# Performance work log

Measured on AMD Instinct MI355X. Metric: run time of the kernel, lower is better.

Reference implementation:

```python
import jax, jax.numpy as jnp
import numpy as np

B, L, C = 2048, 2048, 16
F = L // 2                 # num_freqs = 1024
H = 4 * F                  # multi_factor * num_freqs = 4096
P = int(len(np.unique(L // np.arange(1, F + 1))))  # n patch sizes = 88
SCALE = 0.02
NOISE_EPS = 0.01


def setup_inputs() -> dict:
    key = jax.random.key(0)
    ks = jax.random.split(key, 10)
    return {
        "x": jax.random.normal(ks[0], (B, L, C), jnp.float32),
        "w_start": SCALE * jax.random.normal(ks[1], (C, 1), jnp.float32),
        "b_start": SCALE * jax.random.normal(ks[2], (1,), jnp.float32),
        "w1": SCALE * jax.random.normal(ks[3], (2, F, H), jnp.float32),
        "b1": SCALE * jax.random.normal(ks[4], (2, H), jnp.float32),
        "w2": SCALE * jax.random.normal(ks[5], (2, H, F), jnp.float32),
        "b2": SCALE * jax.random.normal(ks[6], (2, F), jnp.float32),
        "w_gate": SCALE * jax.random.normal(ks[7], (F, P), jnp.float32),
        "w_noise": SCALE * jax.random.normal(ks[8], (F, P), jnp.float32),
        "noise_z": jax.random.normal(ks[9], (B, P), jnp.float32),
        "top_k": 3,
    }


def reference(x, w_start, b_start, w1, b1, w2, b2, w_gate, w_noise, noise_z, top_k):
    # start_fc: [B, L, C] -> [B, L, 1] -> [B, 1, L]
    v = (jnp.einsum("blc,co->blo", x, w_start) + b_start).transpose(0, 2, 1)
    # rfft (ortho), drop DC bin -> [B, 1, F] complex
    xf = jnp.fft.rfft(v, axis=-1, norm="ortho")[:, :, 1:]
    xr, xi = jnp.real(xf), jnp.imag(xf)
    # complex 2-layer MLP in frequency domain
    o1r = jax.nn.relu(jnp.einsum("bdi,io->bdo", xr, w1[0]) - jnp.einsum("bdi,io->bdo", xi, w1[1]) + b1[0])
    o1i = jax.nn.relu(jnp.einsum("bdi,io->bdo", xi, w1[0]) + jnp.einsum("bdi,io->bdo", xr, w1[1]) + b1[1])
    o2r = jnp.einsum("bdo,of->bdf", o1r, w2[0]) - jnp.einsum("bdo,of->bdf", o1i, w2[1]) + b2[0]
    o2i = jnp.einsum("bdo,of->bdf", o1i, w2[0]) + jnp.einsum("bdo,of->bdf", o1r, w2[1]) + b2[1]
    amp = jnp.sqrt(o2r * o2r + o2i * o2i)[:, 0, :]  # [B, F]
    # router logits with (training) noise injection
    clean_logits = amp @ w_gate                      # [B, P]
    noise_std = jax.nn.softplus(amp @ w_noise) + NOISE_EPS
    logits = clean_logits + noise_z * noise_std
    # top-k -> softmax over top-k -> scatter into sparse gates
    top_w, top_i = jax.lax.top_k(logits, top_k)
    top_w = jax.nn.softmax(top_w, axis=-1)
    rows = jnp.arange(logits.shape[0])[:, None]
    gates = jnp.zeros_like(logits).at[rows, top_i].set(top_w)
    return gates
```

## Files before the change

### kernel.cpp

```cpp
#include <hip/hip_runtime.h>
#include <hip/hip_bf16.h>
#include <math.h>

#define B_DIM 2048
#define L_DIM 2048
#define F_DIM 1024
#define H_DIM 4096
#define P_DIM 88

typedef unsigned short u16;
typedef short bf16x8 __attribute__((ext_vector_type(8)));
typedef float f32x4 __attribute__((ext_vector_type(4)));

__device__ __forceinline__ u16 f2bf(float x) {
    unsigned u = __float_as_uint(x);
    return (u16)((u + 0x7fffu + ((u >> 16) & 1u)) >> 16);
}
__device__ __forceinline__ float bf2f(u16 h) {
    return __uint_as_float(((unsigned)h) << 16);
}

__device__ __forceinline__ void gload_lds16(const void* g, void* l) {
    unsigned loff = (unsigned)(uintptr_t)l;
    __builtin_amdgcn_global_load_lds(
        reinterpret_cast<const __attribute__((address_space(1))) void*>(
            reinterpret_cast<uintptr_t>(g)),
        reinterpret_cast<__attribute__((address_space(3))) void*>(loff),
        16, 0, 0);
}

__global__ __launch_bounds__(256) void fft_kernel(
    const float* __restrict__ x, const float* __restrict__ w_start,
    const float* __restrict__ b_start, u16* __restrict__ A1)
{
    __shared__ float re[2048];
    __shared__ float im[2048];
    __shared__ float twr[1024];
    __shared__ float twi[1024];
    int b = blockIdx.x;

    const float4* wp = (const float4*)w_start;
    float4 w0 = wp[0], w1 = wp[1], w2 = wp[2], w3 = wp[3];
    float bs = b_start[0];

    for (int i = threadIdx.x; i < 1024; i += 256) {
        float ang = -6.283185307179586f * ((float)i / 2048.0f);
        sincosf(ang, &twi[i], &twr[i]);
    }

    for (int l = threadIdx.x; l < 2048; l += 256) {
        const float4* xp = (const float4*)(x + ((size_t)b * 2048 + l) * 16);
        float4 x0 = xp[0], x1 = xp[1], x2 = xp[2], x3 = xp[3];
        float acc = bs;
        acc += x0.x * w0.x + x0.y * w0.y + x0.z * w0.z + x0.w * w0.w;
        acc += x1.x * w1.x + x1.y * w1.y + x1.z * w1.z + x1.w * w1.w;
        acc += x2.x * w2.x + x2.y * w2.y + x2.z * w2.z + x2.w * w2.w;
        acc += x3.x * w3.x + x3.y * w3.y + x3.z * w3.z + x3.w * w3.w;
        unsigned j = __brev((unsigned)l) >> 21;
        re[j] = acc;
        im[j] = 0.f;
    }
    __syncthreads();

    for (int s = 1; s <= 11; s++) {
        int half = 1 << (s - 1);
        for (int t = threadIdx.x; t < 1024; t += 256) {
            int j = t & (half - 1);
            int base = (t >> (s - 1)) << s;
            int idx = j << (11 - s);
            float wr = twr[idx], wi = twi[idx];
            int i0 = base + j, i1 = i0 + half;
            float br = re[i1], bi = im[i1];
            float tr = br * wr - bi * wi;
            float ti = br * wi + bi * wr;
            float ar = re[i0], ai = im[i0];
            re[i0] = ar + tr; im[i0] = ai + ti;
            re[i1] = ar - tr; im[i1] = ai - ti;
        }
        __syncthreads();
    }

    const float sc = 0.022097086912079612f;
    u16* arow = A1 + (size_t)b * 4096;
    for (int t = threadIdx.x; t < 1024; t += 256) {
        float r = re[t + 1] * sc;
        float q = im[t + 1] * sc;
        u16 rh = f2bf(r); u16 rl = f2bf(r - bf2f(rh));
        u16 ih = f2bf(q); u16 il = f2bf(q - bf2f(ih));
        arow[t] = rh; arow[1024 + t] = rl;
        arow[2048 + t] = ih; arow[3072 + t] = il;
    }
}

__global__ __launch_bounds__(256) void conv_bt_kernel(
    const float* __restrict__ w, u16* __restrict__ BT, int Kc, int Nh)
{
    __shared__ float t0[32][33];
    __shared__ float t1[32][33];
    int k0 = blockIdx.x * 32, n0 = blockIdx.y * 32;
    int tx = threadIdx.x, ty = threadIdx.y;
    const float* w0 = w;
    const float* w1 = w + (size_t)Kc * Nh;

#pragma unroll
    for (int i = 0; i < 4; i++) {
        int k = k0 + ty + 8 * i;
        t0[ty + 8 * i][tx] = w0[(size_t)k * Nh + n0 + tx];
        t1[ty + 8 * i][tx] = w1[(size_t)k * Nh + n0 + tx];
    }
    __syncthreads();

    size_t K4 = 4 * (size_t)Kc;
    int k = k0 + tx;
#pragma unroll
    for (int i = 0; i < 4; i++) {
        int nl = ty + 8 * i;
        int n = n0 + nl;
        float br = t0[tx][nl];
        float bi = t1[tx][nl];
        u16 brh = f2bf(br); u16 brl = f2bf(br - bf2f(brh));
        float nbi = -bi;
        u16 nih = f2bf(nbi); u16 nil = f2bf(nbi - bf2f(nih));
        u16 pih = f2bf(bi);  u16 pil = f2bf(bi - bf2f(pih));
        u16* rowr = BT + (size_t)n * K4;
        rowr[0 * Kc + k] = brh; rowr[1 * Kc + k] = brl;
        rowr[2 * Kc + k] = nih; rowr[3 * Kc + k] = nil;
        u16* rowi = BT + (size_t)(Nh + n) * K4;
        rowi[0 * Kc + k] = pih; rowi[1 * Kc + k] = pil;
        rowi[2 * Kc + k] = brh; rowi[3 * Kc + k] = brl;
    }
}

extern __shared__ char smem8p[];

#define MFMA16(ACC0, ACC1, ACC2, ACC3, A0, A1, A2, A3, B0, B1, B2, B3)           \
    ACC0[0] = __builtin_amdgcn_mfma_f32_16x16x32_bf16(A0, B0, ACC0[0], 0, 0, 0); \
    ACC0[1] = __builtin_amdgcn_mfma_f32_16x16x32_bf16(A0, B1, ACC0[1], 0, 0, 0); \
    ACC0[2] = __builtin_amdgcn_mfma_f32_16x16x32_bf16(A0, B2, ACC0[2], 0, 0, 0); \
    ACC0[3] = __builtin_amdgcn_mfma_f32_16x16x32_bf16(A0, B3, ACC0[3], 0, 0, 0); \
    ACC1[0] = __builtin_amdgcn_mfma_f32_16x16x32_bf16(A1, B0, ACC1[0], 0, 0, 0); \
    ACC1[1] = __builtin_amdgcn_mfma_f32_16x16x32_bf16(A1, B1, ACC1[1], 0, 0, 0); \
    ACC1[2] = __builtin_amdgcn_mfma_f32_16x16x32_bf16(A1, B2, ACC1[2], 0, 0, 0); \
    ACC1[3] = __builtin_amdgcn_mfma_f32_16x16x32_bf16(A1, B3, ACC1[3], 0, 0, 0); \
    ACC2[0] = __builtin_amdgcn_mfma_f32_16x16x32_bf16(A2, B0, ACC2[0], 0, 0, 0); \
    ACC2[1] = __builtin_amdgcn_mfma_f32_16x16x32_bf16(A2, B1, ACC2[1], 0, 0, 0); \
    ACC2[2] = __builtin_amdgcn_mfma_f32_16x16x32_bf16(A2, B2, ACC2[2], 0, 0, 0); \
    ACC2[3] = __builtin_amdgcn_mfma_f32_16x16x32_bf16(A2, B3, ACC2[3], 0, 0, 0); \
    ACC3[0] = __builtin_amdgcn_mfma_f32_16x16x32_bf16(A3, B0, ACC3[0], 0, 0, 0); \
    ACC3[1] = __builtin_amdgcn_mfma_f32_16x16x32_bf16(A3, B1, ACC3[1], 0, 0, 0); \
    ACC3[2] = __builtin_amdgcn_mfma_f32_16x16x32_bf16(A3, B2, ACC3[2], 0, 0, 0); \
    ACC3[3] = __builtin_amdgcn_mfma_f32_16x16x32_bf16(A3, B3, ACC3[3], 0, 0, 0);

template <int EPI, int SWZ>
__global__ __launch_bounds__(512, 2) void gemm8p(
    const u16* __restrict__ A, const u16* __restrict__ B,
    const float* __restrict__ biasL, const float* __restrict__ biasR,
    u16* __restrict__ OutU, float* __restrict__ P01, float* __restrict__ P23,
    int Kc, int KcLog, int NH, int nt)
{
    char* ldsA = smem8p;
    char* ldsB = smem8p + 65536;

    const int tid = threadIdx.x;
    const int w = tid >> 6, lane = tid & 63;
    const int wr = w >> 2, wc = w & 3;
    const int fr = lane & 15, kb = lane >> 4;

    int bx, by, z;
    if (SWZ) {
        int b = blockIdx.x;
        int xcd = b & 7, idx = b >> 3;
        bx = 4 * xcd + (idx & 3);
        by = idx >> 2;
        z = 0;
    } else {
        bx = blockIdx.x; by = blockIdx.y; z = blockIdx.z;
    }
    const int n0 = bx * 256, m0 = by * 256;
    const size_t K4 = 4 * (size_t)Kc;

    const int srow = tid >> 2;
    const int lk8 = (((tid & 3) ^ ((tid >> 3) & 3))) * 8;
    const int wb = (tid >> 6) * 1024;

    const int laneOff = fr * 64 + ((kb ^ ((fr >> 1) & 3)) << 4);

    f32x4 acc[8][4];
#pragma unroll
    for (int i = 0; i < 8; i++)
#pragma unroll
        for (int j = 0; j < 4; j++)
            acc[i][j] = (f32x4){0.f, 0.f, 0.f, 0.f};

    const int t0 = z * nt, te = t0 + nt;

    auto colA = [&](int t) {
        int k0 = t << 5;
        int seg = k0 >> KcLog, kk = k0 & (Kc - 1);
        int r3 = seg >= 3 ? seg - 3 : seg;
        int bs = seg >= 3 ? 2 : 0;
        return (bs + (r3 == 1 ? 1 : 0)) * Kc + kk;
    };
    auto colB = [&](int t) {
        int k0 = t << 5;
        int seg = k0 >> KcLog, kk = k0 & (Kc - 1);
        int r3 = seg >= 3 ? seg - 3 : seg;
        int bs = seg >= 3 ? 2 : 0;
        return (bs + (r3 == 2 ? 1 : 0)) * Kc + kk;
    };
    auto stageA = [&](int t) {
        const u16* src = A + (size_t)(m0 + srow) * K4 + colA(t) + lk8;
        char* dst = ldsA + (t & 3) * 16384 + wb;
        gload_lds16(src, dst);
        gload_lds16(src + (size_t)128 * K4, dst + 8192);
    };
    auto stageB = [&](int t) {
        const u16* src = B + (size_t)(n0 + srow) * K4 + colB(t) + lk8;
        char* dst = ldsB + (t & 3) * 16384 + wb;
        gload_lds16(src, dst);
        gload_lds16(src + (size_t)128 * K4, dst + 8192);
    };
    auto aBase = [&](int t) -> const char* {
        return ldsA + (t & 3) * 16384 + wr * 8192 + laneOff;
    };
    auto bBase = [&](int t) -> const char* {
        return ldsB + (t & 3) * 16384 + wc * 4096 + laneOff;
    };

    stageA(t0); stageB(t0);
    if (t0 + 1 < te) { stageA(t0 + 1); stageB(t0 + 1); }
    if (t0 + 1 < te) asm volatile("s_waitcnt vmcnt(4)" ::: "memory");
    else             asm volatile("s_waitcnt vmcnt(0)" ::: "memory");
    asm volatile("s_barrier" ::: "memory");

    bf16x8 b0, b1, b2, b3, a0, a1, a2, a3;
    {
        const char* aS = aBase(t0);
        const char* bS = bBase(t0);
        b0 = *(const bf16x8*)(bS + 0 * 1024);
        b1 = *(const bf16x8*)(bS + 1 * 1024);
        b2 = *(const bf16x8*)(bS + 2 * 1024);
        b3 = *(const bf16x8*)(bS + 3 * 1024);
        a0 = *(const bf16x8*)(aS + 0 * 1024);
        a1 = *(const bf16x8*)(aS + 1 * 1024);
        a2 = *(const bf16x8*)(aS + 2 * 1024);
        a3 = *(const bf16x8*)(aS + 3 * 1024);
    }

    for (int t = t0; t < te; ++t) {
        const bool haveStage = (t + 2 < te);
        const bool haveNext  = (t + 1 < te);

        if (haveStage) { stageA(t + 2); stageB(t + 2); }

        const char* aS = aBase(t);
        bf16x8 c0 = *(const bf16x8*)(aS + 4096 + 0 * 1024);
        bf16x8 c1 = *(const bf16x8*)(aS + 4096 + 1 * 1024);
        bf16x8 c2 = *(const bf16x8*)(aS + 4096 + 2 * 1024);
        bf16x8 c3 = *(const bf16x8*)(aS + 4096 + 3 * 1024);

        __builtin_amdgcn_s_setprio(1);
        MFMA16(acc[0], acc[1], acc[2], acc[3], a0, a1, a2, a3, b0, b1, b2, b3)
        __builtin_amdgcn_s_setprio(0);

        if (haveStage) asm volatile("s_waitcnt vmcnt(4)" ::: "memory");
        else           asm volatile("s_waitcnt vmcnt(0)" ::: "memory");
        asm volatile("s_barrier" ::: "memory");

        if (haveNext) {
            const char* aN = aBase(t + 1);
            a0 = *(const bf16x8*)(aN + 0 * 1024);
            a1 = *(const bf16x8*)(aN + 1 * 1024);
            a2 = *(const bf16x8*)(aN + 2 * 1024);
            a3 = *(const bf16x8*)(aN + 3 * 1024);
        }

        __builtin_amdgcn_s_setprio(1);
        MFMA16(acc[4], acc[5], acc[6], acc[7], c0, c1, c2, c3, b0, b1, b2, b3)
        __builtin_amdgcn_s_setprio(0);

        if (haveNext) {
            const char* bN = bBase(t + 1);
            b0 = *(const bf16x8*)(bN + 0 * 1024);
            b1 = *(const bf16x8*)(bN + 1 * 1024);
            b2 = *(const bf16x8*)(bN + 2 * 1024);
            b3 = *(const bf16x8*)(bN + 3 * 1024);
        }
    }

    const int fq = kb;
#pragma unroll
    for (int nj = 0; nj < 4; nj++) {
        int n = n0 + wc * 64 + nj * 16 + fr;
        if (EPI == 0) {
            bool left = (n < NH);
            int nn = left ? n : (n - NH);
            float bias = left ? biasL[n] : biasR[nn];
#pragma unroll
            for (int mi = 0; mi < 8; mi++) {
                int mb = m0 + wr * 128 + mi * 16 + fq * 4;
#pragma unroll
                for (int r = 0; r < 4; r++) {
                    float val = fmaxf(acc[mi][nj][r] + bias, 0.f);
                    u16 h = f2bf(val);
                    u16 lo = f2bf(val - bf2f(h));
                    size_t rb = (size_t)(mb + r) * (4 * (size_t)NH);
                    if (left) { OutU[rb + nn] = h; OutU[rb + NH + nn] = lo; }
                    else { OutU[rb + 2 * (size_t)NH + nn] = h; OutU[rb + 3 * (size_t)NH + nn] = lo; }
                }
            }
        } else {
            const size_t PSZ = (size_t)2048 * 2048;
            float* Out = (z < 2) ? (P01 + (size_t)z * PSZ) : (P23 + (size_t)(z - 2) * PSZ);
#pragma unroll
            for (int mi = 0; mi < 8; mi++) {
                int mb = m0 + wr * 128 + mi * 16 + fq * 4;
#pragma unroll
                for (int r = 0; r < 4; r++)
                    Out[(size_t)(mb + r) * 2048 + n] = acc[mi][nj][r];
            }
        }
    }
}

__global__ __launch_bounds__(128) void router_kernel(
    const float* __restrict__ P01, const float* __restrict__ P23, int ZK,
    const float* __restrict__ b2,
    const float* __restrict__ w_gate, const float* __restrict__ w_noise,
    const float* __restrict__ noise_z, float* __restrict__ gates)
{
    __shared__ float s_amp[1024];
    __shared__ float s_logit[P_DIM];
    __shared__ int   s_idx[3];
    __shared__ float s_val[3];

    int b = blockIdx.x;
    const size_t PSZ = (size_t)2048 * 2048;
    const size_t roff = (size_t)b * 2048;

    for (int i = threadIdx.x; i < 1024; i += 128) {
        float orr = b2[i];
        float oii = b2[1024 + i];
        for (int zz = 0; zz < ZK; zz++) {
            const float* Pz = ((zz < 2) ? (P01 + (size_t)zz * PSZ)
                                        : (P23 + (size_t)(zz - 2) * PSZ)) + roff;
            orr += Pz[i];
            oii += Pz[1024 + i];
        }
        s_amp[i] = sqrtf(orr * orr + oii * oii);
    }
    __syncthreads();

    int p = threadIdx.x;
    if (p < P_DIM) {
        float cg = 0.f, cn = 0.f;
        for (int k = 0; k < 1024; k++) {
            float a = s_amp[k];
            cg = fmaf(a, w_gate[k * P_DIM + p], cg);
            cn = fmaf(a, w_noise[k * P_DIM + p], cn);
        }
        float ns = (cn > 20.f) ? cn : log1pf(expf(cn));
        ns += 0.01f;
        s_logit[p] = cg + noise_z[(size_t)b * P_DIM + p] * ns;
    }
    __syncthreads();

    if (threadIdx.x == 0) {
        int i0 = -1, i1 = -1, i2 = -1;
        float v0 = -1e30f, v1 = -1e30f, v2 = -1e30f;
        for (int i = 0; i < P_DIM; i++) {
            float t = s_logit[i];
            if (t > v0) { v0 = t; i0 = i; }
        }
        for (int i = 0; i < P_DIM; i++) {
            if (i == i0) continue;
            float t = s_logit[i];
            if (t > v1) { v1 = t; i1 = i; }
        }
        for (int i = 0; i < P_DIM; i++) {
            if (i == i0 || i == i1) continue;
            float t = s_logit[i];
            if (t > v2) { v2 = t; i2 = i; }
        }
        s_idx[0] = i0; s_idx[1] = i1; s_idx[2] = i2;
        s_val[0] = v0; s_val[1] = v1; s_val[2] = v2;
    }
    __syncthreads();

    if (p < P_DIM) {
        float m = s_val[0];
        float e0 = expf(s_val[0] - m);
        float e1 = expf(s_val[1] - m);
        float e2 = expf(s_val[2] - m);
        float inv = 1.f / (e0 + e1 + e2);
        float g = 0.f;
        if (p == s_idx[0]) g = e0 * inv;
        else if (p == s_idx[1]) g = e1 * inv;
        else if (p == s_idx[2]) g = e2 * inv;
        gates[(size_t)b * P_DIM + p] = g;
    }
}

extern "C" void kernel_launch(void* const* d_in, const int* in_sizes, int n_in,
                              void* d_out, int out_size, void* d_ws, size_t ws_size,
                              hipStream_t stream)
{
    const float* x       = (const float*)d_in[0];
    const float* w_start = (const float*)d_in[1];
    const float* b_start = (const float*)d_in[2];
    const float* w1      = (const float*)d_in[3];
    const float* b1      = (const float*)d_in[4];
    const float* w2      = (const float*)d_in[5];
    const float* b2      = (const float*)d_in[6];
    const float* w_gate  = (const float*)d_in[7];
    const float* w_noise = (const float*)d_in[8];
    const float* noise_z = (const float*)d_in[9];
    float* gates = (float*)d_out;

    const size_t MB = 1024 * 1024;
    char* base = (char*)d_ws;
    u16*  A1   = (u16*)(base + 16 * MB);
    u16*  BT   = (u16*)(base + 32 * MB);
    u16*  A2   = (u16*)(base + 96 * MB);
    float* P01 = (float*)base;
    float* P23 = (float*)(base + 160 * MB);

    int ZK = (ws_size >= (size_t)192 * MB) ? 4 : 2;

    hipFuncSetAttribute(reinterpret_cast<const void*>(&gemm8p<0, 1>),
                        hipFuncAttributeMaxDynamicSharedMemorySize, 131072);
    hipFuncSetAttribute(reinterpret_cast<const void*>(&gemm8p<1, 0>),
                        hipFuncAttributeMaxDynamicSharedMemorySize, 131072);

    fft_kernel<<<B_DIM, 256, 0, stream>>>(x, w_start, b_start, A1);

    conv_bt_kernel<<<dim3(F_DIM / 32, H_DIM / 32), dim3(32, 8), 0, stream>>>(
        w1, BT, F_DIM, H_DIM);
    gemm8p<0, 1><<<256, 512, 131072, stream>>>(
        A1, BT, b1, b1 + H_DIM, A2, nullptr, nullptr, F_DIM, 10, H_DIM, 192);

    conv_bt_kernel<<<dim3(H_DIM / 32, F_DIM / 32), dim3(32, 8), 0, stream>>>(
        w2, BT, H_DIM, F_DIM);
    gemm8p<1, 0><<<dim3(8, 8, ZK), 512, 131072, stream>>>(
        A2, BT, nullptr, nullptr, nullptr, P01, P23, H_DIM, 12, F_DIM, 768 / ZK);

    router_kernel<<<B_DIM, 128, 0, stream>>>(
        P01, P23, ZK, b2, w_gate, w_noise, noise_z, gates);
}
```

Measured before the change: 598.3 us.

## Pack two real FFTs per complex FFT, restructure GEMM pipeline, batch router rows

The FFT kernel now packs two real input rows into one complex FFT (real and imaginary parts) and separates the two spectra with the conjugate-symmetry trick, halving the FFT block count. The GEMM main loop is reworked so A/B fragments are loaded from LDS at the start of each iteration, with staging of A and B split across the two MFMA halves and extra barriers and lgkmcnt waits. The router kernel processes 8 rows per block and spreads the 176 gate and noise dot products over all threads, which raises thread utilisation and reuses the weight reads across rows. The added barriers and the removal of register prefetch in the GEMM could expose LDS latency.

Result: slower. 634.9 us (+6.1%).

```diff
diff --git a/kernel.cpp b/kernel.cpp
--- a/kernel.cpp
+++ b/kernel.cpp
@@ -38,6 +38,7 @@
     __shared__ float twr[1024];
     __shared__ float twi[1024];
     int b = blockIdx.x;
+    const size_t row0 = (size_t)(2 * b) * 2048;
 
     const float4* wp = (const float4*)w_start;
     float4 w0 = wp[0], w1 = wp[1], w2 = wp[2], w3 = wp[3];
@@ -49,16 +50,22 @@
     }
 
     for (int l = threadIdx.x; l < 2048; l += 256) {
-        const float4* xp = (const float4*)(x + ((size_t)b * 2048 + l) * 16);
-        float4 x0 = xp[0], x1 = xp[1], x2 = xp[2], x3 = xp[3];
-        float acc = bs;
-        acc += x0.x * w0.x + x0.y * w0.y + x0.z * w0.z + x0.w * w0.w;
-        acc += x1.x * w1.x + x1.y * w1.y + x1.z * w1.z + x1.w * w1.w;
-        acc += x2.x * w2.x + x2.y * w2.y + x2.z * w2.z + x2.w * w2.w;
-        acc += x3.x * w3.x + x3.y * w3.y + x3.z * w3.z + x3.w * w3.w;
+        const float4* xp0 = (const float4*)(x + (row0 + l) * 16);
+        const float4* xp1 = (const float4*)(x + (row0 + 2048 + l) * 16);
+        float4 a0 = xp0[0], a1 = xp0[1], a2 = xp0[2], a3 = xp0[3];
+        float4 c0 = xp1[0], c1 = xp1[1], c2 = xp1[2], c3 = xp1[3];
+        float va = bs, vb = bs;
+        va += a0.x * w0.x + a0.y * w0.y + a0.z * w0.z + a0.w * w0.w;
+        va += a1.x * w1.x + a1.y * w1.y + a1.z * w1.z + a1.w * w1.w;
+        va += a2.x * w2.x + a2.y * w2.y + a2.z * w2.z + a2.w * w2.w;
+        va += a3.x * w3.x + a3.y * w3.y + a3.z * w3.z + a3.w * w3.w;
+        vb += c0.x * w0.x + c0.y * w0.y + c0.z * w0.z + c0.w * w0.w;
+        vb += c1.x * w1.x + c1.y * w1.y + c1.z * w1.z + c1.w * w1.w;
+        vb += c2.x * w2.x + c2.y * w2.y + c2.z * w2.z + c2.w * w2.w;
+        vb += c3.x * w3.x + c3.y * w3.y + c3.z * w3.z + c3.w * w3.w;
         unsigned j = __brev((unsigned)l) >> 21;
-        re[j] = acc;
-        im[j] = 0.f;
+        re[j] = va;
+        im[j] = vb;
     }
     __syncthreads();
 
@@ -80,15 +87,22 @@
         __syncthreads();
     }
 
-    const float sc = 0.022097086912079612f;
-    u16* arow = A1 + (size_t)b * 4096;
+    const float sc = 0.5f * 0.022097086912079612f;
+    u16* r0 = A1 + (size_t)(2 * b) * 4096;
+    u16* r1 = r0 + 4096;
     for (int t = threadIdx.x; t < 1024; t += 256) {
-        float r = re[t + 1] * sc;
-        float q = im[t + 1] * sc;
-        u16 rh = f2bf(r); u16 rl = f2bf(r - bf2f(rh));
-        u16 ih = f2bf(q); u16 il = f2bf(q - bf2f(ih));
-        arow[t] = rh; arow[1024 + t] = rl;
-        arow[2048 + t] = ih; arow[3072 + t] = il;
+        int k = t + 1;
+        int nk = 2048 - k;
+        float Zr = re[k], Zi = im[k], Yr = re[nk], Yi = im[nk];
+        float Ar = (Zr + Yr) * sc;
+        float Ai = (Zi - Yi) * sc;
+        float Br = (Zi + Yi) * sc;
+        float Bi = (Yr - Zr) * sc;
+        u16 h, lo;
+        h = f2bf(Ar); lo = f2bf(Ar - bf2f(h)); r0[t] = h; r0[1024 + t] = lo;
+        h = f2bf(Ai); lo = f2bf(Ai - bf2f(h)); r0[2048 + t] = h; r0[3072 + t] = lo;
+        h = f2bf(Br); lo = f2bf(Br - bf2f(h)); r1[t] = h; r1[1024 + t] = lo;
+        h = f2bf(Bi); lo = f2bf(Bi - bf2f(h)); r1[2048 + t] = h; r1[3072 + t] = lo;
     }
 }
 
@@ -228,64 +242,53 @@
     };
 
     stageA(t0); stageB(t0);
-    if (t0 + 1 < te) { stageA(t0 + 1); stageB(t0 + 1); }
-    if (t0 + 1 < te) asm volatile("s_waitcnt vmcnt(4)" ::: "memory");
-    else             asm volatile("s_waitcnt vmcnt(0)" ::: "memory");
+    if (t0 + 1 < te) {
+        stageA(t0 + 1); stageB(t0 + 1);
+        asm volatile("s_waitcnt vmcnt(4)" ::: "memory");
+    } else {
+        asm volatile("s_waitcnt vmcnt(0)" ::: "memory");
+    }
     asm volatile("s_barrier" ::: "memory");
 
-    bf16x8 b0, b1, b2, b3, a0, a1, a2, a3;
-    {
-        const char* aS = aBase(t0);
-        const char* bS = bBase(t0);
-        b0 = *(const bf16x8*)(bS + 0 * 1024);
-        b1 = *(const bf16x8*)(bS + 1 * 1024);
-        b2 = *(const bf16x8*)(bS + 2 * 1024);
-        b3 = *(const bf16x8*)(bS + 3 * 1024);
-        a0 = *(const bf16x8*)(aS + 0 * 1024);
-        a1 = *(const bf16x8*)(aS + 1 * 1024);
-        a2 = *(const bf16x8*)(aS + 2 * 1024);
-        a3 = *(const bf16x8*)(aS + 3 * 1024);
-    }
-
     for (int t = t0; t < te; ++t) {
-        const bool haveStage = (t + 2 < te);
-        const bool haveNext  = (t + 1 < te);
-
-        if (haveStage) { stageA(t + 2); stageB(t + 2); }
-
+        const bool s2 = (t + 2 < te);
         const char* aS = aBase(t);
+        const char* bS = bBase(t);
+
+        bf16x8 a0 = *(const bf16x8*)(aS + 0 * 1024);
+        bf16x8 a1 = *(const bf16x8*)(aS + 1 * 1024);
+        bf16x8 a2 = *(const bf16x8*)(aS + 2 * 1024);
+        bf16x8 a3 = *(const bf16x8*)(aS + 3 * 1024);
+        bf16x8 b0 = *(const bf16x8*)(bS + 0 * 1024);
+        bf16x8 b1 = *(const bf16x8*)(bS + 1 * 1024);
+        bf16x8 b2 = *(const bf16x8*)(bS + 2 * 1024);
+        bf16x8 b3 = *(const bf16x8*)(bS + 3 * 1024);
+        if (s2) stageA(t + 2);
+        asm volatile("s_barrier" ::: "memory");
+        asm volatile("s_waitcnt lgkmcnt(0)" ::: "memory");
+        __builtin_amdgcn_sched_barrier(0);
+        __builtin_amdgcn_s_setprio(1);
+        MFMA16(acc[0], acc[1], acc[2], acc[3], a0, a1, a2, a3, b0, b1, b2, b3)
+        __builtin_amdgcn_s_setprio(0);
+        asm volatile("s_barrier" ::: "memory");
+
         bf16x8 c0 = *(const bf16x8*)(aS + 4096 + 0 * 1024);
         bf16x8 c1 = *(const bf16x8*)(aS + 4096 + 1 * 1024);
         bf16x8 c2 = *(const bf16x8*)(aS + 4096 + 2 * 1024);
         bf16x8 c3 = *(const bf16x8*)(aS + 4096 + 3 * 1024);
-
-        __builtin_amdgcn_s_setprio(1);
-        MFMA16(acc[0], acc[1], acc[2], acc[3], a0, a1, a2, a3, b0, b1, b2, b3)
-        __builtin_amdgcn_s_setprio(0);
-
-        if (haveStage) asm volatile("s_waitcnt vmcnt(4)" ::: "memory");
-        else           asm volatile("s_waitcnt vmcnt(0)" ::: "memory");
+        if (s2) {
+            stageB(t + 2);
+            asm volatile("s_waitcnt vmcnt(4)" ::: "memory");
+        } else {
+            asm volatile("s_waitcnt vmcnt(0)" ::: "memory");
+        }
         asm volatile("s_barrier" ::: "memory");
-
-        if (haveNext) {
-            const char* aN = aBase(t + 1);
-            a0 = *(const bf16x8*)(aN + 0 * 1024);
-            a1 = *(const bf16x8*)(aN + 1 * 1024);
-            a2 = *(const bf16x8*)(aN + 2 * 1024);
-            a3 = *(const bf16x8*)(aN + 3 * 1024);
-        }
-
+        asm volatile("s_waitcnt lgkmcnt(0)" ::: "memory");
+        __builtin_amdgcn_sched_barrier(0);
         __builtin_amdgcn_s_setprio(1);
         MFMA16(acc[4], acc[5], acc[6], acc[7], c0, c1, c2, c3, b0, b1, b2, b3)
         __builtin_amdgcn_s_setprio(0);
-
-        if (haveNext) {
-            const char* bN = bBase(t + 1);
-            b0 = *(const bf16x8*)(bN + 0 * 1024);
-            b1 = *(const bf16x8*)(bN + 1 * 1024);
-            b2 = *(const bf16x8*)(bN + 2 * 1024);
-            b3 = *(const bf16x8*)(bN + 3 * 1024);
-        }
+        asm volatile("s_barrier" ::: "memory");
     }
 
     const int fq = kb;
@@ -323,22 +326,25 @@
     }
 }
 
-__global__ __launch_bounds__(128) void router_kernel(
+__global__ __launch_bounds__(256) void router_kernel(
     const float* __restrict__ P01, const float* __restrict__ P23, int ZK,
     const float* __restrict__ b2,
     const float* __restrict__ w_gate, const float* __restrict__ w_noise,
     const float* __restrict__ noise_z, float* __restrict__ gates)
 {
-    __shared__ float s_amp[1024];
-    __shared__ float s_logit[P_DIM];
-    __shared__ int   s_idx[3];
-    __shared__ float s_val[3];
-
-    int b = blockIdx.x;
+    __shared__ float s_amp[8][1024];
+    __shared__ float s_dot[8][176];
+    __shared__ float s_lg[8][88];
+    __shared__ int   s_idx[8][3];
+    __shared__ float s_val[8][3];
+
+    const int tid = threadIdx.x;
+    const int r0 = blockIdx.x * 8;
     const size_t PSZ = (size_t)2048 * 2048;
-    const size_t roff = (size_t)b * 2048;
-
-    for (int i = threadIdx.x; i < 1024; i += 128) {
+
+    for (int idx = tid; idx < 8 * 1024; idx += 256) {
+        int row = idx >> 10, i = idx & 1023;
+        size_t roff = (size_t)(r0 + row) * 2048;
         float orr = b2[i];
         float oii = b2[1024 + i];
         for (int zz = 0; zz < ZK; zz++) {
@@ -347,57 +353,70 @@
             orr += Pz[i];
             oii += Pz[1024 + i];
         }
-        s_amp[i] = sqrtf(orr * orr + oii * oii);
-    }
-    __syncthreads();
-
-    int p = threadIdx.x;
-    if (p < P_DIM) {
-        float cg = 0.f, cn = 0.f;
-        for (int k = 0; k < 1024; k++) {
-            float a = s_amp[k];
-            cg = fmaf(a, w_gate[k * P_DIM + p], cg);
-            cn = fmaf(a, w_noise[k * P_DIM + p], cn);
-        }
+        s_amp[row][i] = sqrtf(orr * orr + oii * oii);
+    }
+    __syncthreads();
+
+    for (int idx = tid; idx < 8 * 176; idx += 256) {
+        int row = idx / 176, c = idx % 176;
+        const float* wcol = (c < 88) ? (w_gate + c) : (w_noise + (c - 88));
+        float s = 0.f;
+        const float4* av = (const float4*)s_amp[row];
+        for (int k4 = 0; k4 < 256; k4++) {
+            float4 a = av[k4];
+            int k = k4 * 4;
+            s = fmaf(a.x, wcol[(size_t)(k + 0) * 88], s);
+            s = fmaf(a.y, wcol[(size_t)(k + 1) * 88], s);
+            s = fmaf(a.z, wcol[(size_t)(k + 2) * 88], s);
+            s = fmaf(a.w, wcol[(size_t)(k + 3) * 88], s);
+        }
+        s_dot[row][c] = s;
+    }
+    __syncthreads();
+
+    for (int idx = tid; idx < 8 * 88; idx += 256) {
+        int row = idx / 88, c = idx % 88;
+        float cn = s_dot[row][88 + c];
         float ns = (cn > 20.f) ? cn : log1pf(expf(cn));
         ns += 0.01f;
-        s_logit[p] = cg + noise_z[(size_t)b * P_DIM + p] * ns;
-    }
-    __syncthreads();
-
-    if (threadIdx.x == 0) {
+        s_lg[row][c] = s_dot[row][c] + noise_z[(size_t)(r0 + row) * 88 + c] * ns;
+    }
+    __syncthreads();
+
+    if (tid < 8) {
         int i0 = -1, i1 = -1, i2 = -1;
         float v0 = -1e30f, v1 = -1e30f, v2 = -1e30f;
         for (int i = 0; i < P_DIM; i++) {
-            float t = s_logit[i];
+            float t = s_lg[tid][i];
             if (t > v0) { v0 = t; i0 = i; }
         }
         for (int i = 0; i < P_DIM; i++) {
             if (i == i0) continue;
-            float t = s_logit[i];
+            float t = s_lg[tid][i];
             if (t > v1) { v1 = t; i1 = i; }
         }
         for (int i = 0; i < P_DIM; i++) {
             if (i == i0 || i == i1) continue;
-            float t = s_logit[i];
+            float t = s_lg[tid][i];
             if (t > v2) { v2 = t; i2 = i; }
         }
-        s_idx[0] = i0; s_idx[1] = i1; s_idx[2] = i2;
-        s_val[0] = v0; s_val[1] = v1; s_val[2] = v2;
-    }
-    __syncthreads();
-
-    if (p < P_DIM) {
-        float m = s_val[0];
-        float e0 = expf(s_val[0] - m);
-        float e1 = expf(s_val[1] - m);
-        float e2 = expf(s_val[2] - m);
+        s_idx[tid][0] = i0; s_idx[tid][1] = i1; s_idx[tid][2] = i2;
+        s_val[tid][0] = v0; s_val[tid][1] = v1; s_val[tid][2] = v2;
+    }
+    __syncthreads();
+
+    for (int idx = tid; idx < 8 * 88; idx += 256) {
+        int row = idx / 88, c = idx % 88;
+        float m = s_val[row][0];
+        float e0 = expf(s_val[row][0] - m);
+        float e1 = expf(s_val[row][1] - m);
+        float e2 = expf(s_val[row][2] - m);
         float inv = 1.f / (e0 + e1 + e2);
         float g = 0.f;
-        if (p == s_idx[0]) g = e0 * inv;
-        else if (p == s_idx[1]) g = e1 * inv;
-        else if (p == s_idx[2]) g = e2 * inv;
-        gates[(size_t)b * P_DIM + p] = g;
+        if (c == s_idx[row][0]) g = e0 * inv;
+        else if (c == s_idx[row][1]) g = e1 * inv;
+        else if (c == s_idx[row][2]) g = e2 * inv;
+        gates[(size_t)(r0 + row) * 88 + c] = g;
     }
 }
 
@@ -432,7 +451,7 @@
     hipFuncSetAttribute(reinterpret_cast<const void*>(&gemm8p<1, 0>),
                         hipFuncAttributeMaxDynamicSharedMemorySize, 131072);
 
-    fft_kernel<<<B_DIM, 256, 0, stream>>>(x, w_start, b_start, A1);
+    fft_kernel<<<B_DIM / 2, 256, 0, stream>>>(x, w_start, b_start, A1);
 
     conv_bt_kernel<<<dim3(F_DIM / 32, H_DIM / 32), dim3(32, 8), 0, stream>>>(
         w1, BT, F_DIM, H_DIM);
@@ -444,6 +463,6 @@
     gemm8p<1, 0><<<dim3(8, 8, ZK), 512, 131072, stream>>>(
         A2, BT, nullptr, nullptr, nullptr, P01, P23, H_DIM, 12, F_DIM, 768 / ZK);
 
-    router_kernel<<<B_DIM, 128, 0, stream>>>(
+    router_kernel<<<B_DIM / 8, 256, 0, stream>>>(
         P01, P23, ZK, b2, w_gate, w_noise, noise_z, gates);
 }
```
